# Optimization experiments

Hardware: AMD Instinct MI355X
Metric: run time of the kernel (lower is better)

## Reference

```python
import jax, jax.numpy as jnp
import numpy as np

B, T, D, O, E = 4, 4096, 256, 256, 16


def setup_inputs() -> dict:
    key = jax.random.key(0)
    ks = jax.random.split(key, 5)
    s_in = 1.0 / np.sqrt(D)
    x = jax.random.normal(ks[0], (B, T, D), dtype=jnp.float32)
    We = jax.random.uniform(ks[1], (E, D, O), minval=-s_in, maxval=s_in, dtype=jnp.float32)
    be = jax.random.uniform(ks[2], (E, O), minval=-s_in, maxval=s_in, dtype=jnp.float32)
    Wg = jax.random.uniform(ks[3], (D, E), minval=-s_in, maxval=s_in, dtype=jnp.float32)
    bg = jax.random.uniform(ks[4], (E,), minval=-s_in, maxval=s_in, dtype=jnp.float32)
    return {"x": x, "We": We, "be": be, "Wg": Wg, "bg": bg}


def reference(x, We, be, Wg, bg):
    # gate: softmax over experts  [B,T,E]
    gate = jax.nn.softmax(jnp.einsum("btd,de->bte", x, Wg) + bg, axis=-1)
    # all experts: batched GEMM  [B,T,E,O]
    h = jax.nn.gelu(jnp.einsum("btd,edo->bteo", x, We) + be, approximate=False)
    # softmax-weighted sum over experts  [B,T,O]
    return jnp.einsum("bteo,bte->bto", h, gate)
```

## Files before the change

kernel.cpp:

```cpp
#include <hip/hip_runtime.h>
#include <stdint.h>

#define KD 256
#define NO 256
#define NE 16
#define BM 64
#define BN 128
#define XROW 264
#define GROW 68

typedef short bf16x8 __attribute__((ext_vector_type(8)));
typedef float f32x4 __attribute__((ext_vector_type(4)));

__device__ __forceinline__ unsigned short f2bf(float f) {
  uint32_t u = __float_as_uint(f);
  u += 0x7fffu + ((u >> 16) & 1u);
  return (unsigned short)(u >> 16);
}
__device__ __forceinline__ float bf2f(unsigned short h) {
  return __uint_as_float(((uint32_t)h) << 16);
}
__device__ __forceinline__ float gelu_f(float h) {
#if __has_builtin(__builtin_amdgcn_exp2f)
  float zn = h * fmaf(-0.10294817f, h * h, -2.3022077f);
  return h * __builtin_amdgcn_rcpf(1.0f + __builtin_amdgcn_exp2f(zn));
#else
  float z = h * fmaf(0.07135481627f, h * h, 1.5957691216f);
  return h * __builtin_amdgcn_rcpf(1.0f + __expf(-z));
#endif
}

__global__ void moe_prep(const float* __restrict__ We, unsigned short* __restrict__ Wf,
                         const float* __restrict__ Wg, unsigned short* __restrict__ Wgt)
{
  __shared__ float ts[256 * 17];
  const int tid = threadIdx.x;
  const int bid = blockIdx.x;
  if (bid < 256) {
    const int e = bid >> 4, ob = bid & 15;
    const float* src = We + (size_t)e * KD * NO + ob * 16;
    const int o = tid & 15, dg = tid >> 4;
#pragma unroll
    for (int p = 0; p < 16; ++p) {
      int d = p * 16 + dg;
      ts[d * 17 + o] = src[(size_t)d * NO + o];
    }
    __syncthreads();
    const int w = tid >> 6, l = tid & 63;
    const int q = l >> 4, ln = l & 15;
#pragma unroll
    for (int kk = 0; kk < 2; ++kk) {
      int kc = w + kk * 4;
      unsigned int pk[4];
#pragma unroll
      for (int h = 0; h < 4; ++h) {
        unsigned short lo = f2bf(ts[(kc * 32 + q * 8 + h * 2 + 0) * 17 + ln]);
        unsigned short hi = f2bf(ts[(kc * 32 + q * 8 + h * 2 + 1) * 17 + ln]);
        pk[h] = (unsigned int)lo | ((unsigned int)hi << 16);
      }
      uint4* dst = (uint4*)(Wf + ((((size_t)(e * 8 + kc) * 16 + ob) * 64) + l) * 8);
      *dst = make_uint4(pk[0], pk[1], pk[2], pk[3]);
    }
  } else {
    int d = tid;
    const float* wr = Wg + (size_t)d * NE;
#pragma unroll
    for (int e = 0; e < NE; ++e)
      Wgt[e * KD + d] = f2bf(wr[e]);
  }
}

__launch_bounds__(256, 2)
__global__ void moe_main(const float* __restrict__ x,
                         const uint4* __restrict__ Wf,
                         const unsigned short* __restrict__ Wgt,
                         const float* __restrict__ be,
                         const float* __restrict__ bg,
                         float* __restrict__ out)
{
  __shared__ __align__(16) unsigned short Xs[BM * XROW];
  __shared__ __align__(16) float gate_t[NE * GROW];
  __shared__ unsigned short be_h[NE * BN];

  const int tid = threadIdx.x;
  const int bid = blockIdx.x;
  const int half = bid & 1;
  const int n0 = half * BN;
  const int m0 = (bid >> 1) * BM;
  const int w = tid >> 6, lane = tid & 63;
  const int ln = lane & 15, quad = lane >> 4;
  const int eoff = __builtin_amdgcn_readfirstlane(((tid >> 6) * 4 + bid) & 15);

  const int voff = (half * 8 + w * 2) * 64 + lane;

  {
    const float4* xg = (const float4*)x + (size_t)m0 * (KD / 4);
#pragma unroll
    for (int p = 0; p < 16; ++p) {
      int idx = p * 256 + tid;
      int r = idx >> 6, c = idx & 63;
      float4 v = xg[r * (KD / 4) + c];
      uint32_t lo = (uint32_t)f2bf(v.x) | ((uint32_t)f2bf(v.y) << 16);
      uint32_t hi = (uint32_t)f2bf(v.z) | ((uint32_t)f2bf(v.w) << 16);
      *(uint2*)&Xs[r * XROW + c * 4] = make_uint2(lo, hi);
    }
  }
  uint4 bbA[8], bbB[8];
  {
    const uint4* p0 = Wf + (size_t)eoff * 8192 + voff;
#pragma unroll
    for (int kc = 0; kc < 8; ++kc) bbA[kc] = p0[kc * 1024];
  }
#pragma unroll
  for (int p = 0; p < 8; ++p) {
    int idx = p * 256 + tid;
    int e = idx >> 7, c = idx & 127;
    be_h[e * BN + c] = f2bf(be[e * NO + n0 + c]);
  }
  __syncthreads();

  bf16x8 a[4][8];
#pragma unroll
  for (int i = 0; i < 4; ++i)
#pragma unroll
    for (int kc = 0; kc < 8; ++kc)
      a[i][kc] = *(const bf16x8*)&Xs[(i * 16 + ln) * XROW + kc * 32 + quad * 8];

  {
    f32x4 g = {0.f, 0.f, 0.f, 0.f};
#pragma unroll
    for (int kc = 0; kc < 8; ++kc) {
      bf16x8 af = *(const bf16x8*)&Xs[(w * 16 + ln) * XROW + kc * 32 + quad * 8];
      bf16x8 wb = *(const bf16x8*)(Wgt + (size_t)ln * KD + kc * 32 + quad * 8);
      g = __builtin_amdgcn_mfma_f32_16x16x32_bf16(af, wb, g, 0, 0, 0);
    }
    float bgl = bg[ln];
#pragma unroll
    for (int r = 0; r < 4; ++r) {
      float v = g[r] + bgl;
      float mx = v;
#pragma unroll
      for (int msk = 1; msk < 16; msk <<= 1)
        mx = fmaxf(mx, __shfl_xor(mx, msk, 64));
      float ev = __expf(v - mx);
      float s = ev;
#pragma unroll
      for (int msk = 1; msk < 16; msk <<= 1)
        s += __shfl_xor(s, msk, 64);
      gate_t[ln * GROW + w * 16 + quad * 4 + r] = ev * __builtin_amdgcn_rcpf(s);
    }
  }
  __syncthreads();

  f32x4 oacc[4][2];
#pragma unroll
  for (int i = 0; i < 4; ++i)
#pragma unroll
    for (int j = 0; j < 2; ++j)
      oacc[i][j] = (f32x4){0.f, 0.f, 0.f, 0.f};

#pragma unroll 1
  for (int ei = 0; ei < NE; ++ei) {
    const int e  = (eoff + ei) & 15;
    const int en = (eoff + ei + 1) & 15;
    const uint4* __restrict__ bse = Wf + (size_t)e  * 8192 + voff;
    const uint4* __restrict__ bsn = Wf + (size_t)en * 8192 + voff;
    const float bb0 = bf2f(be_h[e * BN + w * 32 + ln]);
    const float bb1 = bf2f(be_h[e * BN + w * 32 + 16 + ln]);

#pragma unroll
    for (int kc = 0; kc < 8; ++kc) bbB[kc] = bse[kc * 1024 + 64];
#pragma unroll
    for (int i = 0; i < 4; ++i) {
      f32x4 gvq = *(const f32x4*)&gate_t[e * GROW + i * 16 + quad * 4];
      f32x4 acc = {0.f, 0.f, 0.f, 0.f};
#pragma unroll
      for (int kc = 0; kc < 8; ++kc)
        acc = __builtin_amdgcn_mfma_f32_16x16x32_bf16(
            a[i][kc], *(const bf16x8*)&bbA[kc], acc, 0, 0, 0);
#pragma unroll
      for (int r = 0; r < 4; ++r) {
        float hh = acc[r] + bb0;
        oacc[i][0][r] = fmaf(gvq[r], gelu_f(hh), oacc[i][0][r]);
      }
    }

#pragma unroll
    for (int kc = 0; kc < 8; ++kc) bbA[kc] = bsn[kc * 1024];
#pragma unroll
    for (int i = 0; i < 4; ++i) {
      f32x4 gvq = *(const f32x4*)&gate_t[e * GROW + i * 16 + quad * 4];
      f32x4 acc = {0.f, 0.f, 0.f, 0.f};
#pragma unroll
      for (int kc = 0; kc < 8; ++kc)
        acc = __builtin_amdgcn_mfma_f32_16x16x32_bf16(
            a[i][kc], *(const bf16x8*)&bbB[kc], acc, 0, 0, 0);
#pragma unroll
      for (int r = 0; r < 4; ++r) {
        float hh = acc[r] + bb1;
        oacc[i][1][r] = fmaf(gvq[r], gelu_f(hh), oacc[i][1][r]);
      }
    }
  }

#pragma unroll
  for (int i = 0; i < 4; ++i)
#pragma unroll
    for (int r = 0; r < 4; ++r) {
      int row = m0 + i * 16 + quad * 4 + r;
      float* orow = out + (size_t)row * NO + n0 + w * 32 + ln;
      orow[0]  = oacc[i][0][r];
      orow[16] = oacc[i][1][r];
    }
}

extern "C" void kernel_launch(void* const* d_in, const int* in_sizes, int n_in,
                              void* d_out, int out_size, void* d_ws, size_t ws_size,
                              hipStream_t stream) {
  const float* x  = (const float*)d_in[0];
  const float* We = (const float*)d_in[1];
  const float* be = (const float*)d_in[2];
  const float* Wg = (const float*)d_in[3];
  const float* bg = (const float*)d_in[4];
  float* out = (float*)d_out;
  unsigned short* Wf  = (unsigned short*)d_ws;
  unsigned short* Wgt = (unsigned short*)((char*)d_ws + (size_t)NE * NO * KD * 2);

  moe_prep<<<257, 256, 0, stream>>>(We, Wf, Wg, Wgt);
  moe_main<<<512, 256, 0, stream>>>(x, (const uint4*)Wf, Wgt, be, bg, out);
}
```

Before: 124.8 us.

## Software-pipeline expert GEMMs so GELU epilogue overlaps next tile's MFMAs

Replaces the double B-register buffers with a single 8-entry buffer that is refilled slot-by-slot as each k-chunk is consumed. The MFMA loop is reordered to iterate kc outer and row-tile inner, giving four independent accumulators. The loop gets a prologue and epilogue so the GELU/gate epilogue for one half-tile runs after the MFMAs of the other half are issued, letting the two overlap. This saves B registers but adds live accumulator registers (accA/accB) and longer code, which may pressure occupancy under the 2-wave launch bound.

```diff
diff --git a/kernel.cpp b/kernel.cpp
--- a/kernel.cpp
+++ b/kernel.cpp
@@ -105,11 +105,12 @@
       *(uint2*)&Xs[r * XROW + c * 4] = make_uint2(lo, hi);
     }
   }
-  uint4 bbA[8], bbB[8];
+  uint4 b8[8];
   {
     const uint4* p0 = Wf + (size_t)eoff * 8192 + voff;
 #pragma unroll
-    for (int kc = 0; kc < 8; ++kc) bbA[kc] = p0[kc * 1024];
+    for (int kc = 0; kc < 8; ++kc)
+      b8[kc] = p0[kc * 1024];
   }
 #pragma unroll
   for (int p = 0; p < 8; ++p) {
@@ -152,53 +153,98 @@
   }
   __syncthreads();
 
+  f32x4 accA[4], accB[4];
   f32x4 oacc[4][2];
 #pragma unroll
-  for (int i = 0; i < 4; ++i)
-#pragma unroll
-    for (int j = 0; j < 2; ++j)
-      oacc[i][j] = (f32x4){0.f, 0.f, 0.f, 0.f};
+  for (int i = 0; i < 4; ++i) {
+    oacc[i][0] = (f32x4){0.f, 0.f, 0.f, 0.f};
+    oacc[i][1] = (f32x4){0.f, 0.f, 0.f, 0.f};
+  }
+
+  {
+    const uint4* __restrict__ bse = Wf + (size_t)eoff * 8192 + voff;
+#pragma unroll
+    for (int i = 0; i < 4; ++i) accA[i] = (f32x4){0.f, 0.f, 0.f, 0.f};
+#pragma unroll
+    for (int kc = 0; kc < 8; ++kc) {
+#pragma unroll
+      for (int i = 0; i < 4; ++i)
+        accA[i] = __builtin_amdgcn_mfma_f32_16x16x32_bf16(
+            a[i][kc], *(const bf16x8*)&b8[kc], accA[i], 0, 0, 0);
+      b8[kc] = bse[kc * 1024 + 64];
+    }
+  }
 
 #pragma unroll 1
-  for (int ei = 0; ei < NE; ++ei) {
+  for (int ei = 0; ei < NE - 1; ++ei) {
     const int e  = (eoff + ei) & 15;
     const int en = (eoff + ei + 1) & 15;
-    const uint4* __restrict__ bse = Wf + (size_t)e  * 8192 + voff;
     const uint4* __restrict__ bsn = Wf + (size_t)en * 8192 + voff;
     const float bb0 = bf2f(be_h[e * BN + w * 32 + ln]);
     const float bb1 = bf2f(be_h[e * BN + w * 32 + 16 + ln]);
 
 #pragma unroll
-    for (int kc = 0; kc < 8; ++kc) bbB[kc] = bse[kc * 1024 + 64];
+    for (int i = 0; i < 4; ++i) accB[i] = (f32x4){0.f, 0.f, 0.f, 0.f};
+#pragma unroll
+    for (int kc = 0; kc < 8; ++kc) {
+#pragma unroll
+      for (int i = 0; i < 4; ++i)
+        accB[i] = __builtin_amdgcn_mfma_f32_16x16x32_bf16(
+            a[i][kc], *(const bf16x8*)&b8[kc], accB[i], 0, 0, 0);
+      b8[kc] = bsn[kc * 1024];
+    }
 #pragma unroll
     for (int i = 0; i < 4; ++i) {
-      f32x4 gvq = *(const f32x4*)&gate_t[e * GROW + i * 16 + quad * 4];
-      f32x4 acc = {0.f, 0.f, 0.f, 0.f};
-#pragma unroll
-      for (int kc = 0; kc < 8; ++kc)
-        acc = __builtin_amdgcn_mfma_f32_16x16x32_bf16(
-            a[i][kc], *(const bf16x8*)&bbA[kc], acc, 0, 0, 0);
+      const f32x4 gq = *(const f32x4*)&gate_t[e * GROW + i * 16 + quad * 4];
 #pragma unroll
       for (int r = 0; r < 4; ++r) {
-        float hh = acc[r] + bb0;
-        oacc[i][0][r] = fmaf(gvq[r], gelu_f(hh), oacc[i][0][r]);
-      }
-    }
-
-#pragma unroll
-    for (int kc = 0; kc < 8; ++kc) bbA[kc] = bsn[kc * 1024];
+        float hh = accA[i][r] + bb0;
+        oacc[i][0][r] = fmaf(gq[r], gelu_f(hh), oacc[i][0][r]);
+      }
+    }
+
+#pragma unroll
+    for (int i = 0; i < 4; ++i) accA[i] = (f32x4){0.f, 0.f, 0.f, 0.f};
+#pragma unroll
+    for (int kc = 0; kc < 8; ++kc) {
+#pragma unroll
+      for (int i = 0; i < 4; ++i)
+        accA[i] = __builtin_amdgcn_mfma_f32_16x16x32_bf16(
+            a[i][kc], *(const bf16x8*)&b8[kc], accA[i], 0, 0, 0);
+      b8[kc] = bsn[kc * 1024 + 64];
+    }
 #pragma unroll
     for (int i = 0; i < 4; ++i) {
-      f32x4 gvq = *(const f32x4*)&gate_t[e * GROW + i * 16 + quad * 4];
-      f32x4 acc = {0.f, 0.f, 0.f, 0.f};
-#pragma unroll
-      for (int kc = 0; kc < 8; ++kc)
-        acc = __builtin_amdgcn_mfma_f32_16x16x32_bf16(
-            a[i][kc], *(const bf16x8*)&bbB[kc], acc, 0, 0, 0);
+      const f32x4 gq = *(const f32x4*)&gate_t[e * GROW + i * 16 + quad * 4];
 #pragma unroll
       for (int r = 0; r < 4; ++r) {
-        float hh = acc[r] + bb1;
-        oacc[i][1][r] = fmaf(gvq[r], gelu_f(hh), oacc[i][1][r]);
+        float hh = accB[i][r] + bb1;
+        oacc[i][1][r] = fmaf(gq[r], gelu_f(hh), oacc[i][1][r]);
+      }
+    }
+  }
+
+  {
+    const int e = (eoff + NE - 1) & 15;
+    const float bb0 = bf2f(be_h[e * BN + w * 32 + ln]);
+    const float bb1 = bf2f(be_h[e * BN + w * 32 + 16 + ln]);
+#pragma unroll
+    for (int i = 0; i < 4; ++i) accB[i] = (f32x4){0.f, 0.f, 0.f, 0.f};
+#pragma unroll
+    for (int kc = 0; kc < 8; ++kc)
+#pragma unroll
+      for (int i = 0; i < 4; ++i)
+        accB[i] = __builtin_amdgcn_mfma_f32_16x16x32_bf16(
+            a[i][kc], *(const bf16x8*)&b8[kc], accB[i], 0, 0, 0);
+#pragma unroll
+    for (int i = 0; i < 4; ++i) {
+      const f32x4 gq = *(const f32x4*)&gate_t[e * GROW + i * 16 + quad * 4];
+#pragma unroll
+      for (int r = 0; r < 4; ++r) {
+        float h0 = accA[i][r] + bb0;
+        oacc[i][0][r] = fmaf(gq[r], gelu_f(h0), oacc[i][0][r]);
+        float h1 = accB[i][r] + bb1;
+        oacc[i][1][r] = fmaf(gq[r], gelu_f(h1), oacc[i][1][r]);
       }
     }
   }
```

New measurement: 121.7 us. -2.5%, faster.
